# Kernel optimization log

Measured on AMD Instinct MI355X. Metric: run time of the kernel, lower is better.

Reference implementation:

```python
import jax, jax.numpy as jnp
import numpy as np

N_NODES = 50000
N_EDGES = 640000
F_IN = 64
EDGE_DIM = 16
HID = 128
N_LAYERS = 3
N_CLASSES = 2
NUM_GRAPHS = 64
BN_EPS = 1e-5


def setup_inputs() -> dict:
    key = jax.random.key(0)
    ks = jax.random.split(key, 20)
    s = 0.05
    inp = {
        "x": jax.random.normal(ks[0], (N_NODES, F_IN), dtype=jnp.float32),
        "edge_index": jax.random.randint(ks[1], (2, N_EDGES), 0, N_NODES, dtype=jnp.int32),
        "edge_attr": jax.random.normal(ks[2], (N_EDGES, EDGE_DIM), dtype=jnp.float32),
        "batch": jnp.sort(jax.random.randint(ks[3], (N_NODES,), 0, NUM_GRAPHS, dtype=jnp.int32)),
        # node encoder
        "enc_W": jax.random.normal(ks[4], (F_IN, HID), dtype=jnp.float32) * s,
        "enc_b": jnp.zeros((HID,), dtype=jnp.float32),
        # per-layer GINEConv params (stacked over layers)
        "edge_W": jax.random.normal(ks[5], (N_LAYERS, EDGE_DIM, HID), dtype=jnp.float32) * s,
        "edge_b": jnp.zeros((N_LAYERS, HID), dtype=jnp.float32),
        "mlp_W1": jax.random.normal(ks[6], (N_LAYERS, HID, HID), dtype=jnp.float32) * s,
        "mlp_b1": jnp.zeros((N_LAYERS, HID), dtype=jnp.float32),
        "mlp_W2": jax.random.normal(ks[7], (N_LAYERS, HID, HID), dtype=jnp.float32) * s,
        "mlp_b2": jnp.zeros((N_LAYERS, HID), dtype=jnp.float32),
        "bn_gamma": jnp.ones((N_LAYERS, HID), dtype=jnp.float32),
        "bn_beta": jnp.zeros((N_LAYERS, HID), dtype=jnp.float32),
        # classification head
        "head_W1": jax.random.normal(ks[8], (HID, HID), dtype=jnp.float32) * s,
        "head_b1": jnp.zeros((HID,), dtype=jnp.float32),
        "head_W2": jax.random.normal(ks[9], (HID, N_CLASSES), dtype=jnp.float32) * s,
        "head_b2": jnp.zeros((N_CLASSES,), dtype=jnp.float32),
    }
    return inp


def reference(x, edge_index, edge_attr, batch, enc_W, enc_b, edge_W, edge_b,
              mlp_W1, mlp_b1, mlp_W2, mlp_b2, bn_gamma, bn_beta,
              head_W1, head_b1, head_W2, head_b2):
    src, dst = edge_index[0], edge_index[1]  # message flows src -> dst
    h = x @ enc_W + enc_b  # [N, HID]
    for l in range(N_LAYERS):
        # GINEConv: msg = ReLU(x_src + Lin(edge_attr)); aggr = scatter_add at dst
        e = edge_attr @ edge_W[l] + edge_b[l]          # [E, HID]
        msg = jax.nn.relu(h[src] + e)                  # [E, HID]
        agg = jax.ops.segment_sum(msg, dst, num_segments=N_NODES)
        z = h + agg  # (1 + eps) * x + aggr, eps = 0
        # node MLP: Linear-ReLU-Linear
        z = jax.nn.relu(z @ mlp_W1[l] + mlp_b1[l]) @ mlp_W2[l] + mlp_b2[l]
        # BatchNorm1d (training-mode batch stats) + ReLU (dropout = identity)
        mean = jnp.mean(z, axis=0)
        var = jnp.var(z, axis=0)
        z = bn_gamma[l] * (z - mean) * jax.lax.rsqrt(var + BN_EPS) + bn_beta[l]
        h = jax.nn.relu(z)
    # global_add_pool over graphs
    g = jax.ops.segment_sum(h, batch, num_segments=NUM_GRAPHS)  # [G, HID]
    out = jax.nn.relu(g @ head_W1 + head_b1) @ head_W2 + head_b2
    return out  # [G, N_CLASSES]
```

## Files before the change

kernel.cpp:

```cpp
#include <hip/hip_runtime.h>
#include <hip/hip_bf16.h>

#define N_NODES 50000
#define N_EDGES 640000
#define F_IN 64
#define EDGE_DIM 16
#define HID 128
#define N_LAYERS 3
#define NUM_GRAPHS 64
#define BN_EPS 1e-5f

typedef __attribute__((ext_vector_type(8))) short short8;
typedef __attribute__((ext_vector_type(4))) float f32x4;
typedef __attribute__((ext_vector_type(2))) __fp16 half2v;
typedef __attribute__((ext_vector_type(8))) __fp16 half8;

__device__ __forceinline__ float bfl(unsigned int u) {
    unsigned int v = u << 16; float f; __builtin_memcpy(&f, &v, 4); return f;
}
__device__ __forceinline__ float bfh(unsigned int u) {
    unsigned int v = u & 0xffff0000u; float f; __builtin_memcpy(&f, &v, 4); return f;
}
__device__ __forceinline__ unsigned int f2bf(float f) {
    unsigned int v; __builtin_memcpy(&v, &f, 4);
    v += 0x7fffu + ((v >> 16) & 1u);
    return v >> 16;
}
__device__ __forceinline__ unsigned int pack2(float lo, float hi) {
    return f2bf(lo) | (f2bf(hi) << 16);
}
__device__ __forceinline__ unsigned int pkh(float a, float b) {
    half2v h = __builtin_amdgcn_cvt_pkrtz(a, b);
    unsigned int u; __builtin_memcpy(&u, &h, 4); return u;
}

__global__ void k_hist(const int* __restrict__ dst, int* __restrict__ deg) {
    int e = blockIdx.x * 256 + threadIdx.x;
    atomicAdd(&deg[dst[e]], 1);
}

__global__ void k_blockred(const int* __restrict__ deg, int* __restrict__ bsums) {
    __shared__ int s[256];
    int i = blockIdx.x * 256 + threadIdx.x;
    int v = (i < N_NODES) ? deg[i] : 0;
    s[threadIdx.x] = v;
    __syncthreads();
    for (int off = 128; off > 0; off >>= 1) {
        if (threadIdx.x < off) s[threadIdx.x] += s[threadIdx.x + off];
        __syncthreads();
    }
    if (threadIdx.x == 0) bsums[blockIdx.x] = s[0];
}

__global__ void k_scan_bsums(int* __restrict__ bsums, int nb) {
    __shared__ int s[256];
    const int tid = threadIdx.x;
    const int v = (tid < nb) ? bsums[tid] : 0;
    s[tid] = v;
    __syncthreads();
    for (int off = 1; off < 256; off <<= 1) {
        int t = 0;
        if (tid >= off) t = s[tid - off];
        __syncthreads();
        s[tid] += t;
        __syncthreads();
    }
    if (tid < nb) bsums[tid] = s[tid] - v;
}

__global__ void k_scan_blocks(int* __restrict__ deg_rowptr, const int* __restrict__ bsums,
                              int* __restrict__ cursor) {
    __shared__ int s[256];
    int tid = threadIdx.x;
    int i = blockIdx.x * 256 + tid;
    int v = (i < N_NODES) ? deg_rowptr[i] : 0;
    s[tid] = v;
    __syncthreads();
    for (int off = 1; off < 256; off <<= 1) {
        int t = 0;
        if (tid >= off) t = s[tid - off];
        __syncthreads();
        s[tid] += t;
        __syncthreads();
    }
    int excl = s[tid] - v + bsums[blockIdx.x];
    if (i < N_NODES) {
        deg_rowptr[i] = excl;
        cursor[i] = excl;
    }
    if (i == N_NODES - 1) deg_rowptr[N_NODES] = N_EDGES;
}

__global__ void k_fill(const int* __restrict__ dst, int* __restrict__ cursor,
                       int* __restrict__ elist) {
    int e = blockIdx.x * 256 + threadIdx.x;
    int p = atomicAdd(&cursor[dst[e]], 1);
    elist[p] = e;
}

__global__ __launch_bounds__(256) void k_gather(const int* __restrict__ elist,
                                                const int* __restrict__ esrc,
                                                const float* __restrict__ eattr,
                                                int* __restrict__ src_s,
                                                uint4* __restrict__ eattr_h) {
    const int base = blockIdx.x * 1024;
    const int tid = threadIdx.x;
    int p[4], eid[4];
#pragma unroll
    for (int j = 0; j < 4; ++j) p[j] = base + tid + j * 256;
#pragma unroll
    for (int j = 0; j < 4; ++j) eid[j] = elist[p[j]];
    int sv[4];
#pragma unroll
    for (int j = 0; j < 4; ++j) sv[j] = esrc[eid[j]];
    float4 a[4][4];
#pragma unroll
    for (int j = 0; j < 4; ++j) {
        const float* ep = eattr + (size_t)eid[j] * EDGE_DIM;
        a[j][0] = *(const float4*)ep;
        a[j][1] = *(const float4*)(ep + 4);
        a[j][2] = *(const float4*)(ep + 8);
        a[j][3] = *(const float4*)(ep + 12);
    }
#pragma unroll
    for (int j = 0; j < 4; ++j) {
        src_s[p[j]] = sv[j];
        eattr_h[p[j] * 2] = make_uint4(pkh(a[j][0].x, a[j][0].y), pkh(a[j][0].z, a[j][0].w),
                                       pkh(a[j][1].x, a[j][1].y), pkh(a[j][1].z, a[j][1].w));
        eattr_h[p[j] * 2 + 1] = make_uint4(pkh(a[j][2].x, a[j][2].y), pkh(a[j][2].z, a[j][2].w),
                                           pkh(a[j][3].x, a[j][3].y), pkh(a[j][3].z, a[j][3].w));
    }
}

__global__ void k_pack(const float* __restrict__ W1, const float* __restrict__ W2,
                       const float* __restrict__ encW, const float* __restrict__ eW,
                       const float* __restrict__ eb2,
                       unsigned short* __restrict__ wp, unsigned short* __restrict__ wpe,
                       unsigned short* __restrict__ wekf) {
    const int t = blockIdx.x * 256 + threadIdx.x;
    if (t < 12288) {
        const int mat = t >> 11;
        const int r = t & 2047;
        const int kstep = r >> 9;
        const int ntile = (r >> 6) & 7;
        const int lane = r & 63;
        const float* W = (mat < 3) ? (W1 + mat * 16384) : (W2 + (mat - 3) * 16384);
        const int kbase = kstep * 32 + ((lane >> 4) << 3);
        const int n = ntile * 16 + (lane & 15);
        unsigned int o[4];
#pragma unroll
        for (int jj = 0; jj < 4; ++jj)
            o[jj] = pack2(W[(kbase + 2 * jj) * HID + n], W[(kbase + 2 * jj + 1) * HID + n]);
        *(uint4*)(wp + (size_t)mat * 16384 + (((kstep << 3) + ntile) * 64 + lane) * 8) =
            make_uint4(o[0], o[1], o[2], o[3]);
    } else if (t < 13312) {
        const int r = t - 12288;
        const int kstep = r >> 9;
        const int ntile = (r >> 6) & 7;
        const int lane = r & 63;
        const int kbase = kstep * 32 + ((lane >> 4) << 3);
        const int n = ntile * 16 + (lane & 15);
        unsigned int o[4];
#pragma unroll
        for (int jj = 0; jj < 4; ++jj)
            o[jj] = pack2(encW[(kbase + 2 * jj) * HID + n], encW[(kbase + 2 * jj + 1) * HID + n]);
        *(uint4*)(wpe + (((kstep << 3) + ntile) * 64 + lane) * 8) =
            make_uint4(o[0], o[1], o[2], o[3]);
    } else {
        const int r = t - 13312;
        const int l = r >> 10;
        const int rr = r & 1023;
        const int nt = rr >> 7;
        const int lane = (rr >> 1) & 63;
        const int hf = rr & 1;
        const int qq = lane >> 4;
        const int f = ((lane & 15) << 3) + nt;
        float v[4];
#pragma unroll
        for (int j = 0; j < 4; ++j) {
            const int k = (qq << 3) + (hf << 2) + j;
            v[j] = (k < 16) ? eW[(l * EDGE_DIM + k) * HID + f]
                            : ((k == 16) ? eb2[l * HID + f] : 0.f);
        }
        *(uint2*)(wekf + (((l * 8 + nt) * 64 + lane) * 8) + (hf << 2)) =
            make_uint2(pkh(v[0], v[1]), pkh(v[2], v[3]));
    }
}

__global__ __launch_bounds__(256, 3) void k_encm(const float* __restrict__ x,
                                                 const unsigned short* __restrict__ wpe,
                                                 const float* __restrict__ b,
                                                 unsigned short* __restrict__ hb) {
    const int tid = threadIdx.x;
    const int w = tid >> 6, lane = tid & 63;
    const int q = lane >> 4, l15 = lane & 15;
    const int row0 = blockIdx.x * 64 + w * 16;
    const int ar = min(row0 + l15, N_NODES - 1);
    const float* xp = x + (size_t)ar * F_IN + q * 8;
    f32x4 acc[8];
#pragma unroll
    for (int nt = 0; nt < 8; ++nt) acc[nt] = (f32x4){0.f, 0.f, 0.f, 0.f};
#pragma unroll
    for (int ks = 0; ks < 2; ++ks) {
        const float4 v0 = *(const float4*)(xp + ks * 32);
        const float4 v1 = *(const float4*)(xp + ks * 32 + 4);
        unsigned int u[4] = {pack2(v0.x, v0.y), pack2(v0.z, v0.w),
                             pack2(v1.x, v1.y), pack2(v1.z, v1.w)};
        short8 a; __builtin_memcpy(&a, u, 16);
#pragma unroll
        for (int nt = 0; nt < 8; ++nt) {
            const short8 bf = *(const short8*)(wpe + (((ks << 3) + nt) * 64 + lane) * 8);
            acc[nt] = __builtin_amdgcn_mfma_f32_16x16x32_bf16(a, bf, acc[nt], 0, 0, 0);
        }
    }
    const int rowb = row0 + q * 4;
#pragma unroll
    for (int nt = 0; nt < 8; ++nt) {
        const float bias = b[nt * 16 + l15];
        const int cc = nt * 16 + l15;
#pragma unroll
        for (int reg = 0; reg < 4; ++reg) {
            const int r = rowb + reg;
            if (r < N_NODES)
                hb[(size_t)r * HID + cc] = (unsigned short)f2bf(acc[nt][reg] + bias);
        }
    }
}

__global__ __launch_bounds__(256) void k_bn(const unsigned short* __restrict__ z,
                                            const float* __restrict__ bnst,
                                            const float* __restrict__ gamma,
                                            const float* __restrict__ beta,
                                            unsigned short* __restrict__ hb2) {
    const int idx = blockIdx.x * 256 + threadIdx.x;
    const int f0 = (idx * 8) & 127;
    const float invN = 1.0f / (float)N_NODES;
    uint4 v = *(const uint4*)(z + (size_t)idx * 8);
    const unsigned int* u = (const unsigned int*)&v;
    unsigned int o[4];
#pragma unroll
    for (int p = 0; p < 4; ++p) {
        const int f = f0 + 2 * p;
        const float m0 = bnst[f] * invN;
        const float m1 = bnst[f + 1] * invN;
        const float v0 = fmaxf(bnst[128 + f] * invN - m0 * m0, 0.f);
        const float v1 = fmaxf(bnst[128 + f + 1] * invN - m1 * m1, 0.f);
        const float r0 = rsqrtf(v0 + BN_EPS), r1 = rsqrtf(v1 + BN_EPS);
        const float sc0 = gamma[f] * r0, sc1 = gamma[f + 1] * r1;
        const float sh0 = fmaf(-m0, sc0, beta[f]);
        const float sh1 = fmaf(-m1, sc1, beta[f + 1]);
        const float a = fmaxf(fmaf(bfl(u[p]), sc0, sh0), 0.f);
        const float b = fmaxf(fmaf(bfh(u[p]), sc1, sh1), 0.f);
        o[p] = pack2(a, b);
    }
    *(uint4*)(hb2 + (size_t)idx * 8) = make_uint4(o[0], o[1], o[2], o[3]);
}

__global__ __launch_bounds__(256, 4) void k_agg(const unsigned short* __restrict__ hrow,
                                                const int* __restrict__ src_s,
                                                const uint4* __restrict__ eattr_h,
                                                const unsigned short* __restrict__ wekf,
                                                const int* __restrict__ row_ptr,
                                                unsigned int* __restrict__ zb32) {
    const int lane = threadIdx.x & 63;
    const int wv = threadIdx.x >> 6;
    const int q = lane >> 4, l15 = lane & 15;
    const int f0 = l15 * 8;

    half8 Bf[8];
#pragma unroll
    for (int nt = 0; nt < 8; ++nt) {
        uint4 u = *(const uint4*)(wekf + (nt * 64 + lane) * 8);
        __builtin_memcpy(&Bf[nt], &u, 16);
    }

    const int w0 = blockIdx.x * 4 + wv;

    for (int n = w0; n < N_NODES; n += 8192) {
        const int base = __builtin_amdgcn_readfirstlane(row_ptr[n]);
        const int deg  = __builtin_amdgcn_readfirstlane(row_ptr[n + 1]) - base;

        float accf[8];
#pragma unroll
        for (int j = 0; j < 8; ++j) accf[j] = 0.f;

        if (deg > 0) {
            const int ntile = (deg + 15) >> 4;
            for (int t = 0; t < ntile; ++t) {
                const int e0 = t * 16;
                uint4 au = make_uint4(0u, 0u, 0u, 0u);
                if (q < 2) {
                    const int ea = min(e0 + l15, deg - 1);
                    au = eattr_h[(size_t)(base + ea) * 2 + q];
                } else if (q == 2) {
                    au.x = 0x3C00u;
                }
                half8 Af; __builtin_memcpy(&Af, &au, 16);

                int sv[4];
#pragma unroll
                for (int r = 0; r < 4; ++r)
                    sv[r] = src_s[base + min(e0 + q * 4 + r, deg - 1)];
                uint4 hg[4];
#pragma unroll
                for (int r = 0; r < 4; ++r)
                    hg[r] = *(const uint4*)(hrow + (size_t)sv[r] * HID + f0);

                f32x4 acc[8];
#pragma unroll
                for (int nt = 0; nt < 8; ++nt) {
                    acc[nt] = (f32x4){0.f, 0.f, 0.f, 0.f};
                    acc[nt] = __builtin_amdgcn_mfma_f32_16x16x32_f16(Af, Bf[nt], acc[nt], 0, 0, 0);
                }

#pragma unroll
                for (int r = 0; r < 4; ++r) {
                    const float m = (e0 + q * 4 + r < deg) ? 1.f : 0.f;
                    const unsigned int* hu = (const unsigned int*)&hg[r];
#pragma unroll
                    for (int p = 0; p < 4; ++p) {
                        accf[2 * p]     = fmaf(m, fmaxf(bfl(hu[p]) + acc[2 * p][r],     0.f), accf[2 * p]);
                        accf[2 * p + 1] = fmaf(m, fmaxf(bfh(hu[p]) + acc[2 * p + 1][r], 0.f), accf[2 * p + 1]);
                    }
                }
            }
        }

#pragma unroll
        for (int j = 0; j < 8; ++j) {
            accf[j] += __shfl_xor(accf[j], 16, 64);
            accf[j] += __shfl_xor(accf[j], 32, 64);
        }

        if (q == 0) {
            const uint4 hs = *(const uint4*)(hrow + (size_t)n * HID + f0);
            const unsigned int* hu = (const unsigned int*)&hs;
            unsigned int o[4];
#pragma unroll
            for (int p = 0; p < 4; ++p)
                o[p] = pack2(bfl(hu[p]) + accf[2 * p], bfh(hu[p]) + accf[2 * p + 1]);
            *(uint4*)(zb32 + (size_t)n * 64 + l15 * 4) = make_uint4(o[0], o[1], o[2], o[3]);
        }
    }
}

#define Z1LD 136

__global__ __launch_bounds__(256, 3) void k_mlp(const unsigned short* __restrict__ zb,
                                                const unsigned short* __restrict__ w1p,
                                                const float* __restrict__ b1,
                                                const unsigned short* __restrict__ w2p,
                                                const float* __restrict__ b2,
                                                unsigned short* __restrict__ z2b,
                                                float* __restrict__ bn) {
    __shared__ unsigned short z1s[64 * Z1LD];
    __shared__ float redA[512];
    __shared__ float redB[512];
    const int tid = threadIdx.x;
    const int w = tid >> 6, lane = tid & 63;
    const int q = lane >> 4, l15 = lane & 15;
    const int row0 = blockIdx.x * 64 + w * 16;

    const int ar = min(row0 + l15, N_NODES - 1);
    const unsigned short* aptr = zb + (size_t)ar * HID + q * 8;

    f32x4 acc[8];
#pragma unroll
    for (int nt = 0; nt < 8; ++nt) acc[nt] = (f32x4){0.f, 0.f, 0.f, 0.f};

#pragma unroll
    for (int ks = 0; ks < 4; ++ks) {
        const short8 a = *(const short8*)(aptr + ks * 32);
#pragma unroll
        for (int nt = 0; nt < 8; ++nt) {
            const short8 b = *(const short8*)(w1p + (((ks << 3) + nt) * 64 + lane) * 8);
            acc[nt] = __builtin_amdgcn_mfma_f32_16x16x32_bf16(a, b, acc[nt], 0, 0, 0);
        }
    }
    {
        const int lr0 = w * 16 + q * 4;
#pragma unroll
        for (int nt = 0; nt < 8; ++nt) {
            const float bias = b1[nt * 16 + l15];
            const int cc = nt * 16 + l15;
#pragma unroll
            for (int reg = 0; reg < 4; ++reg) {
                const float v = fmaxf(acc[nt][reg] + bias, 0.f);
                z1s[(lr0 + reg) * Z1LD + cc] = (unsigned short)f2bf(v);
            }
        }
    }
#pragma unroll
    for (int nt = 0; nt < 8; ++nt) acc[nt] = (f32x4){0.f, 0.f, 0.f, 0.f};
    const unsigned short* a2p = &z1s[(w * 16 + l15) * Z1LD + q * 8];
#pragma unroll
    for (int ks = 0; ks < 4; ++ks) {
        const short8 a = *(const short8*)(a2p + ks * 32);
#pragma unroll
        for (int nt = 0; nt < 8; ++nt) {
            const short8 b = *(const short8*)(w2p + (((ks << 3) + nt) * 64 + lane) * 8);
            acc[nt] = __builtin_amdgcn_mfma_f32_16x16x32_bf16(a, b, acc[nt], 0, 0, 0);
        }
    }
    float s[8], sq[8];
    const int rowb = row0 + q * 4;
#pragma unroll
    for (int nt = 0; nt < 8; ++nt) {
        const float bias = b2[nt * 16 + l15];
        const int cc = nt * 16 + l15;
        float ls = 0.f, lq = 0.f;
#pragma unroll
        for (int reg = 0; reg < 4; ++reg) {
            const int r = rowb + reg;
            const float v = acc[nt][reg] + bias;
            if (r < N_NODES) {
                z2b[(size_t)r * HID + cc] = (unsigned short)f2bf(v);
                ls += v;
                lq = fmaf(v, v, lq);
            }
        }
        s[nt] = ls; sq[nt] = lq;
    }
#pragma unroll
    for (int nt = 0; nt < 8; ++nt) {
        s[nt] += __shfl_xor(s[nt], 16, 64);
        s[nt] += __shfl_xor(s[nt], 32, 64);
        sq[nt] += __shfl_xor(sq[nt], 16, 64);
        sq[nt] += __shfl_xor(sq[nt], 32, 64);
    }
    if (lane < 16) {
#pragma unroll
        for (int nt = 0; nt < 8; ++nt) {
            redA[w * 128 + nt * 16 + lane] = s[nt];
            redB[w * 128 + nt * 16 + lane] = sq[nt];
        }
    }
    __syncthreads();
    if (tid < 128) {
        float t = redA[tid] + redA[128 + tid] + redA[256 + tid] + redA[384 + tid];
        atomicAdd(&bn[tid], t);
    } else {
        const int c = tid - 128;
        float t = redB[c] + redB[128 + c] + redB[256 + c] + redB[384 + c];
        atomicAdd(&bn[128 + c], t);
    }
}

__global__ void k_pool(const unsigned short* __restrict__ z2b, const int* __restrict__ batch,
                       const float* __restrict__ bnst, const float* __restrict__ gamma,
                       const float* __restrict__ beta, float* __restrict__ g) {
    const int f = threadIdx.x;
    const float invN = 1.0f / (float)N_NODES;
    const float m = bnst[f] * invN;
    const float var = fmaxf(bnst[128 + f] * invN - m * m, 0.f);
    const float r = rsqrtf(var + BN_EPS);
    const float sc = gamma[f] * r;
    const float sh = fmaf(-m, sc, beta[f]);

    const int n0 = blockIdx.x * 128;
    const int nend = min(n0 + 128, N_NODES);
    float acc = 0.f;
    int cur = batch[n0];
    for (int n = n0; n < nend; ++n) {
        const int bb = batch[n];
        if (bb != cur) {
            atomicAdd(&g[cur * HID + f], acc);
            acc = 0.f;
            cur = bb;
        }
        const float raw = bfl((unsigned int)z2b[n * HID + f]);
        acc += fmaxf(fmaf(raw, sc, sh), 0.f);
    }
    atomicAdd(&g[cur * HID + f], acc);
}

__global__ void k_head1(const float* __restrict__ g, const float* __restrict__ W,
                        const float* __restrict__ b, float* __restrict__ g1) {
    const int idx = blockIdx.x * 256 + threadIdx.x;
    const int r = idx >> 7, c = idx & 127;
    float acc = b[c];
    for (int k = 0; k < 128; ++k) acc = fmaf(g[r * HID + k], W[k * HID + c], acc);
    g1[idx] = fmaxf(acc, 0.f);
}

__global__ void k_head2(const float* __restrict__ g1, const float* __restrict__ W,
                        const float* __restrict__ b, float* __restrict__ out) {
    const int idx = threadIdx.x;
    const int r = idx >> 1, c = idx & 1;
    float acc = b[c];
    for (int k = 0; k < 128; ++k) acc = fmaf(g1[r * HID + k], W[k * 2 + c], acc);
    out[idx] = acc;
}

extern "C" void kernel_launch(void* const* d_in, const int* in_sizes, int n_in,
                              void* d_out, int out_size, void* d_ws, size_t ws_size,
                              hipStream_t stream) {
    const float* x     = (const float*)d_in[0];
    const int*   ei    = (const int*)d_in[1];
    const float* eattr = (const float*)d_in[2];
    const int*   batch = (const int*)d_in[3];
    const float* encW  = (const float*)d_in[4];
    const float* encb  = (const float*)d_in[5];
    const float* eW    = (const float*)d_in[6];
    const float* eb    = (const float*)d_in[7];
    const float* W1    = (const float*)d_in[8];
    const float* b1    = (const float*)d_in[9];
    const float* W2    = (const float*)d_in[10];
    const float* b2    = (const float*)d_in[11];
    const float* gam   = (const float*)d_in[12];
    const float* bet   = (const float*)d_in[13];
    const float* hW1   = (const float*)d_in[14];
    const float* hb1   = (const float*)d_in[15];
    const float* hW2   = (const float*)d_in[16];
    const float* hb2w  = (const float*)d_in[17];
    float* out = (float*)d_out;

    float* ws = (float*)d_ws;
    unsigned short* z2b = (unsigned short*)ws;
    float* bn  = ws + 3200000;
    float* g   = ws + 3200256;
    float* g1  = ws + 3208448;
    unsigned short* hb  = (unsigned short*)(ws + 3216640);
    unsigned int* zb32  = (unsigned int*)(ws + 6416640);
    unsigned short* hb2 = (unsigned short*)(ws + 9616640);
    unsigned short* wekf = (unsigned short*)(ws + 12816640);
    unsigned short* wp  = (unsigned short*)(ws + 12822784);
    unsigned short* wpe = (unsigned short*)(ws + 12871936);
    int* row_ptr = (int*)(ws + 12876032);
    int* cursor  = row_ptr + N_NODES + 1;
    int* elist   = cursor + N_NODES;
    int* bsums   = elist + N_EDGES;
    int* src_s   = bsums + 256;
    uint4* eattr_h = (uint4*)(ws + 14256292);

    const int* esrc = ei;
    const int* edst = ei + N_EDGES;

    hipMemsetAsync(row_ptr, 0, (N_NODES + 1) * sizeof(int), stream);
    k_hist<<<N_EDGES / 256, 256, 0, stream>>>(edst, row_ptr);
    k_blockred<<<196, 256, 0, stream>>>(row_ptr, bsums);
    k_scan_bsums<<<1, 256, 0, stream>>>(bsums, 196);
    k_scan_blocks<<<196, 256, 0, stream>>>(row_ptr, bsums, cursor);
    k_fill<<<N_EDGES / 256, 256, 0, stream>>>(edst, cursor, elist);
    k_gather<<<N_EDGES / 1024, 256, 0, stream>>>(elist, esrc, eattr, src_s, eattr_h);

    k_pack<<<64, 256, 0, stream>>>(W1, W2, encW, eW, eb, wp, wpe, wekf);

    k_encm<<<782, 256, 0, stream>>>(x, wpe, encb, hb);

    for (int l = 0; l < N_LAYERS; ++l) {
        const unsigned short* hrow;
        if (l == 0) {
            hrow = hb;
        } else {
            k_bn<<<3125, 256, 0, stream>>>(z2b, bn, gam + (l - 1) * HID,
                                           bet + (l - 1) * HID, hb2);
            hrow = hb2;
        }
        k_agg<<<2048, 256, 0, stream>>>(hrow, src_s, eattr_h,
                                        wekf + (size_t)l * 4096, row_ptr, zb32);
        hipMemsetAsync(bn, 0, 256 * sizeof(float), stream);
        k_mlp<<<782, 256, 0, stream>>>((const unsigned short*)zb32,
                                       wp + (size_t)l * 16384, b1 + l * HID,
                                       wp + (size_t)(3 + l) * 16384, b2 + l * HID,
                                       z2b, bn);
    }

    hipMemsetAsync(g, 0, NUM_GRAPHS * HID * sizeof(float), stream);
    k_pool<<<391, 128, 0, stream>>>(z2b, batch, bn, gam + 2 * HID, bet + 2 * HID, g);
    k_head1<<<32, 256, 0, stream>>>(g, hW1, hb1, g1);
    k_head2<<<1, 128, 0, stream>>>(g1, hW2, hb2w, out);
}
```

Before: 524.7 us.

## Switch node activations from bf16 to fp16 with packed-half aggregation

Node features, intermediate MLP activations and packed MLP weights move from bf16 to fp16, and the MLP matmuls use fp16 MFMA instructions. The edge-aggregation inner loop now adds, applies ReLU and accumulates in packed half2 arithmetic, replacing per-element fp32 FMAs with masking. This halves the ALU work and register pressure in the gather-heavy aggregation kernel. The cost is fp16 accumulation over many edges, which risks precision loss or overflow for high-degree nodes and large activations.

```diff
diff --git a/kernel.cpp b/kernel.cpp
--- a/kernel.cpp
+++ b/kernel.cpp
@@ -15,12 +15,6 @@
 typedef __attribute__((ext_vector_type(2))) __fp16 half2v;
 typedef __attribute__((ext_vector_type(8))) __fp16 half8;
 
-__device__ __forceinline__ float bfl(unsigned int u) {
-    unsigned int v = u << 16; float f; __builtin_memcpy(&f, &v, 4); return f;
-}
-__device__ __forceinline__ float bfh(unsigned int u) {
-    unsigned int v = u & 0xffff0000u; float f; __builtin_memcpy(&f, &v, 4); return f;
-}
 __device__ __forceinline__ unsigned int f2bf(float f) {
     unsigned int v; __builtin_memcpy(&v, &f, 4);
     v += 0x7fffu + ((v >> 16) & 1u);
@@ -32,6 +26,20 @@
 __device__ __forceinline__ unsigned int pkh(float a, float b) {
     half2v h = __builtin_amdgcn_cvt_pkrtz(a, b);
     unsigned int u; __builtin_memcpy(&u, &h, 4); return u;
+}
+__device__ __forceinline__ unsigned short f2h(float f) {
+    return (unsigned short)(pkh(f, 0.f) & 0xffffu);
+}
+__device__ __forceinline__ float f16l(unsigned int u) {
+    unsigned short s = (unsigned short)(u & 0xffffu);
+    _Float16 h; __builtin_memcpy(&h, &s, 2); return (float)h;
+}
+__device__ __forceinline__ float f16h(unsigned int u) {
+    unsigned short s = (unsigned short)(u >> 16);
+    _Float16 h; __builtin_memcpy(&h, &s, 2); return (float)h;
+}
+__device__ __forceinline__ half2v u2h(unsigned int u) {
+    half2v h; __builtin_memcpy(&h, &u, 4); return h;
 }
 
 __global__ void k_hist(const int* __restrict__ dst, int* __restrict__ deg) {
@@ -150,7 +158,7 @@
         unsigned int o[4];
 #pragma unroll
         for (int jj = 0; jj < 4; ++jj)
-            o[jj] = pack2(W[(kbase + 2 * jj) * HID + n], W[(kbase + 2 * jj + 1) * HID + n]);
+            o[jj] = pkh(W[(kbase + 2 * jj) * HID + n], W[(kbase + 2 * jj + 1) * HID + n]);
         *(uint4*)(wp + (size_t)mat * 16384 + (((kstep << 3) + ntile) * 64 + lane) * 8) =
             make_uint4(o[0], o[1], o[2], o[3]);
     } else if (t < 13312) {
@@ -222,7 +230,7 @@
         for (int reg = 0; reg < 4; ++reg) {
             const int r = rowb + reg;
             if (r < N_NODES)
-                hb[(size_t)r * HID + cc] = (unsigned short)f2bf(acc[nt][reg] + bias);
+                hb[(size_t)r * HID + cc] = f2h(acc[nt][reg] + bias);
         }
     }
 }
@@ -249,9 +257,9 @@
         const float sc0 = gamma[f] * r0, sc1 = gamma[f + 1] * r1;
         const float sh0 = fmaf(-m0, sc0, beta[f]);
         const float sh1 = fmaf(-m1, sc1, beta[f + 1]);
-        const float a = fmaxf(fmaf(bfl(u[p]), sc0, sh0), 0.f);
-        const float b = fmaxf(fmaf(bfh(u[p]), sc1, sh1), 0.f);
-        o[p] = pack2(a, b);
+        const float a = fmaxf(fmaf(f16l(u[p]), sc0, sh0), 0.f);
+        const float b = fmaxf(fmaf(f16h(u[p]), sc1, sh1), 0.f);
+        o[p] = pkh(a, b);
     }
     *(uint4*)(hb2 + (size_t)idx * 8) = make_uint4(o[0], o[1], o[2], o[3]);
 }
@@ -266,6 +274,7 @@
     const int wv = threadIdx.x >> 6;
     const int q = lane >> 4, l15 = lane & 15;
     const int f0 = l15 * 8;
+    const half2v zero2 = {(__fp16)0.f, (__fp16)0.f};
 
     half8 Bf[8];
 #pragma unroll
@@ -280,9 +289,9 @@
         const int base = __builtin_amdgcn_readfirstlane(row_ptr[n]);
         const int deg  = __builtin_amdgcn_readfirstlane(row_ptr[n + 1]) - base;
 
-        float accf[8];
-#pragma unroll
-        for (int j = 0; j < 8; ++j) accf[j] = 0.f;
+        half2v accp[4];
+#pragma unroll
+        for (int j = 0; j < 4; ++j) accp[j] = zero2;
 
         if (deg > 0) {
             const int ntile = (deg + 15) >> 4;
@@ -315,21 +324,27 @@
 
 #pragma unroll
                 for (int r = 0; r < 4; ++r) {
-                    const float m = (e0 + q * 4 + r < deg) ? 1.f : 0.f;
+                    const bool valid = (e0 + q * 4 + r < deg);
                     const unsigned int* hu = (const unsigned int*)&hg[r];
 #pragma unroll
                     for (int p = 0; p < 4; ++p) {
-                        accf[2 * p]     = fmaf(m, fmaxf(bfl(hu[p]) + acc[2 * p][r],     0.f), accf[2 * p]);
-                        accf[2 * p + 1] = fmaf(m, fmaxf(bfh(hu[p]) + acc[2 * p + 1][r], 0.f), accf[2 * p + 1]);
+                        half2v e2 = __builtin_amdgcn_cvt_pkrtz(acc[2 * p][r], acc[2 * p + 1][r]);
+                        half2v s2 = u2h(hu[p]) + e2;
+                        s2 = __builtin_elementwise_max(s2, zero2);
+                        s2 = valid ? s2 : zero2;
+                        accp[p] = accp[p] + s2;
                     }
                 }
             }
         }
 
 #pragma unroll
-        for (int j = 0; j < 8; ++j) {
-            accf[j] += __shfl_xor(accf[j], 16, 64);
-            accf[j] += __shfl_xor(accf[j], 32, 64);
+        for (int j = 0; j < 4; ++j) {
+            unsigned int u;
+            __builtin_memcpy(&u, &accp[j], 4);
+            accp[j] = accp[j] + u2h((unsigned int)__shfl_xor((int)u, 16, 64));
+            __builtin_memcpy(&u, &accp[j], 4);
+            accp[j] = accp[j] + u2h((unsigned int)__shfl_xor((int)u, 32, 64));
         }
 
         if (q == 0) {
@@ -337,8 +352,10 @@
             const unsigned int* hu = (const unsigned int*)&hs;
             unsigned int o[4];
 #pragma unroll
-            for (int p = 0; p < 4; ++p)
-                o[p] = pack2(bfl(hu[p]) + accf[2 * p], bfh(hu[p]) + accf[2 * p + 1]);
+            for (int p = 0; p < 4; ++p) {
+                half2v z2 = u2h(hu[p]) + accp[p];
+                __builtin_memcpy(&o[p], &z2, 4);
+            }
             *(uint4*)(zb32 + (size_t)n * 64 + l15 * 4) = make_uint4(o[0], o[1], o[2], o[3]);
         }
     }
@@ -370,11 +387,11 @@
 
 #pragma unroll
     for (int ks = 0; ks < 4; ++ks) {
-        const short8 a = *(const short8*)(aptr + ks * 32);
+        const half8 a = *(const half8*)(aptr + ks * 32);
 #pragma unroll
         for (int nt = 0; nt < 8; ++nt) {
-            const short8 b = *(const short8*)(w1p + (((ks << 3) + nt) * 64 + lane) * 8);
-            acc[nt] = __builtin_amdgcn_mfma_f32_16x16x32_bf16(a, b, acc[nt], 0, 0, 0);
+            const half8 b = *(const half8*)(w1p + (((ks << 3) + nt) * 64 + lane) * 8);
+            acc[nt] = __builtin_amdgcn_mfma_f32_16x16x32_f16(a, b, acc[nt], 0, 0, 0);
         }
     }
     {
@@ -386,7 +403,7 @@
 #pragma unroll
             for (int reg = 0; reg < 4; ++reg) {
                 const float v = fmaxf(acc[nt][reg] + bias, 0.f);
-                z1s[(lr0 + reg) * Z1LD + cc] = (unsigned short)f2bf(v);
+                z1s[(lr0 + reg) * Z1LD + cc] = f2h(v);
             }
         }
     }
@@ -395,11 +412,11 @@
     const unsigned short* a2p = &z1s[(w * 16 + l15) * Z1LD + q * 8];
 #pragma unroll
     for (int ks = 0; ks < 4; ++ks) {
-        const short8 a = *(const short8*)(a2p + ks * 32);
+        const half8 a = *(const half8*)(a2p + ks * 32);
 #pragma unroll
         for (int nt = 0; nt < 8; ++nt) {
-            const short8 b = *(const short8*)(w2p + (((ks << 3) + nt) * 64 + lane) * 8);
-            acc[nt] = __builtin_amdgcn_mfma_f32_16x16x32_bf16(a, b, acc[nt], 0, 0, 0);
+            const half8 b = *(const half8*)(w2p + (((ks << 3) + nt) * 64 + lane) * 8);
+            acc[nt] = __builtin_amdgcn_mfma_f32_16x16x32_f16(a, b, acc[nt], 0, 0, 0);
         }
     }
     float s[8], sq[8];
@@ -414,7 +431,7 @@
             const int r = rowb + reg;
             const float v = acc[nt][reg] + bias;
             if (r < N_NODES) {
-                z2b[(size_t)r * HID + cc] = (unsigned short)f2bf(v);
+                z2b[(size_t)r * HID + cc] = f2h(v);
                 ls += v;
                 lq = fmaf(v, v, lq);
             }
@@ -468,7 +485,7 @@
             acc = 0.f;
             cur = bb;
         }
-        const float raw = bfl((unsigned int)z2b[n * HID + f]);
+        const float raw = f16l((unsigned int)z2b[n * HID + f]);
         acc += fmaxf(fmaf(raw, sc, sh), 0.f);
     }
     atomicAdd(&g[cur * HID + f], acc);
```

Measured after the change: 544.9 us. 1.04x slower.
